# Kernel optimization log

Hardware: AMD Instinct MI355X
Metric: run time of the kernel (lower is better)

Reference implementation:

```python
import jax, jax.numpy as jnp
import numpy as np


def setup_inputs() -> dict:
    key = jax.random.key(0)
    ks = jax.random.split(key, 8)
    B, T, V, H = 32, 256, 1024, 1024
    scale_i = 1.0 / np.sqrt(V)   # lecun_normal-style init for dense kernels
    scale_h = 1.0 / np.sqrt(H)
    return {
        "c0": jax.random.normal(ks[0], (B, H), jnp.float32),
        "h0": jax.random.normal(ks[1], (B, H), jnp.float32),
        "inputs": jax.random.normal(ks[2], (B, T, V), jnp.float32),
        "Wi": jax.random.normal(ks[3], (V, 4 * H), jnp.float32) * scale_i,
        "Wh": jax.random.normal(ks[4], (H, 4 * H), jnp.float32) * scale_h,
        "b": jnp.zeros((4 * H,), jnp.float32),
        "Wd": jax.random.normal(ks[5], (H, V), jnp.float32) * scale_h,
        "bd": jnp.zeros((V,), jnp.float32),
    }


def reference(c0, h0, inputs, Wi, Wh, b, Wd, bd):
    # LSTM scanned over time axis (axis=1 of inputs), then Dense -> vocab.
    H = h0.shape[-1]

    def step(carry, x_t):  # x_t: [B, V]
        c, h = carry
        z = x_t @ Wi + h @ Wh + b            # [B, 4H], gates i,f,g,o
        i, f, g, o = jnp.split(z, 4, axis=-1)
        i = jax.nn.sigmoid(i)
        f = jax.nn.sigmoid(f)
        g = jnp.tanh(g)
        o = jax.nn.sigmoid(o)
        c = f * c + i * g
        h = o * jnp.tanh(c)
        return (c, h), h

    xs = jnp.swapaxes(inputs, 0, 1)          # [T, B, V]
    (c, h), hs = jax.lax.scan(step, (c0, h0), xs)
    outputs = jnp.swapaxes(hs, 0, 1)          # [B, T, H]
    x = outputs @ Wd + bd                     # [B, T, V]
    return (c, h, x)
```

## Files before the change

kernel.cpp:

```cpp
#include <hip/hip_runtime.h>
#include <cstdio>

typedef unsigned short u16;
typedef unsigned int u32;
typedef unsigned long long u64;
typedef __attribute__((ext_vector_type(8))) short bf16x8;
typedef __attribute__((ext_vector_type(4))) float f32x4;

#define NWG 128
#define FLAG_STRIDE 32

__device__ inline u16 f2bf(float x) {
  union { float f; unsigned u; } v; v.f = x;
  unsigned r = v.u + 0x7FFFu + ((v.u >> 16) & 1u);
  return (u16)(r >> 16);
}
__device__ inline float sigm(float x) { return 1.0f / (1.0f + __expf(-x)); }
__device__ inline float tanh_fast(float x) { return 1.0f - 2.0f / (__expf(2.0f * x) + 1.0f); }

__global__ __launch_bounds__(256) void k_convert(const float* __restrict__ in,
                                                 u16* __restrict__ out, int n4) {
  int i = blockIdx.x * blockDim.x + threadIdx.x;
  int stride = gridDim.x * blockDim.x;
  const float4* in4 = (const float4*)in;
  ushort4* out4 = (ushort4*)out;
  for (; i < n4; i += stride) {
    float4 v = in4[i];
    ushort4 o; o.x = f2bf(v.x); o.y = f2bf(v.y); o.z = f2bf(v.z); o.w = f2bf(v.w);
    out4[i] = o;
  }
}

__global__ __launch_bounds__(256) void k_init_h(const float* __restrict__ h0,
                                                u16* __restrict__ h_bf,
                                                u32* __restrict__ flags) {
  int i = blockIdx.x * blockDim.x + threadIdx.x;
  if (i < NWG * FLAG_STRIDE) flags[i] = 0u;
  if (i < 32768) h_bf[i] = f2bf(h0[i]);
}

__global__ __launch_bounds__(256) void k_transpose(const float* __restrict__ in,
                                                   u16* __restrict__ out, int R, int C) {
  __shared__ u16 tile[32][33];
  int tx = threadIdx.x & 31, ty = threadIdx.x >> 5;
  int c = blockIdx.x * 32 + tx;
  for (int i = 0; i < 32; i += 8) {
    int r = blockIdx.y * 32 + ty + i;
    tile[ty + i][tx] = f2bf(in[(size_t)r * C + c]);
  }
  __syncthreads();
  int r = blockIdx.y * 32 + tx;
  for (int i = 0; i < 32; i += 8) {
    int cc = blockIdx.x * 32 + ty + i;
    out[(size_t)cc * R + r] = tile[tx][ty + i];
  }
}

__global__ __launch_bounds__(256) void k_gemm_bt(const u16* __restrict__ A,
                                                 const u16* __restrict__ BT,
                                                 const float* __restrict__ bias,
                                                 float* __restrict__ C,
                                                 int M, int N, int K) {
  __shared__ u16 As[128][40];
  __shared__ u16 Bs[128][40];
  const int m0 = blockIdx.y * 128, n0 = blockIdx.x * 128;
  const int tid = threadIdx.x;
  const int lane = tid & 63, wave = tid >> 6;
  const int wm = (wave >> 1) * 64, wn = (wave & 1) * 64;
  const int lm = lane & 15, quad = lane >> 4;
  const int r = tid >> 1, kh = (tid & 1) * 16;

  f32x4 acc[4][4];
  for (int i = 0; i < 4; i++)
    for (int j = 0; j < 4; j++) acc[i][j] = (f32x4){0.f, 0.f, 0.f, 0.f};

  for (int k0 = 0; k0 < K; k0 += 32) {
    const uint4* ap = (const uint4*)(A + (size_t)(m0 + r) * K + k0 + kh);
    uint4 av0 = ap[0], av1 = ap[1];
    const uint4* bp = (const uint4*)(BT + (size_t)(n0 + r) * K + k0 + kh);
    uint4 bv0 = bp[0], bv1 = bp[1];
    __syncthreads();
    *(uint4*)&As[r][kh] = av0; *(uint4*)&As[r][kh + 8] = av1;
    *(uint4*)&Bs[r][kh] = bv0; *(uint4*)&Bs[r][kh + 8] = bv1;
    __syncthreads();
    bf16x8 a_frag[4], b_frag[4];
    for (int i = 0; i < 4; i++) a_frag[i] = *(const bf16x8*)&As[wm + i * 16 + lm][quad * 8];
    for (int j = 0; j < 4; j++) b_frag[j] = *(const bf16x8*)&Bs[wn + j * 16 + lm][quad * 8];
    for (int i = 0; i < 4; i++)
      for (int j = 0; j < 4; j++)
        acc[i][j] = __builtin_amdgcn_mfma_f32_16x16x32_bf16(a_frag[i], b_frag[j], acc[i][j], 0, 0, 0);
  }
  for (int i = 0; i < 4; i++)
    for (int j = 0; j < 4; j++) {
      int row = m0 + wm + i * 16 + quad * 4;
      int col = n0 + wn + j * 16 + lm;
      float bc = bias[col];
      for (int rr = 0; rr < 4; rr++)
        C[(size_t)(row + rr) * N + col] = acc[i][j][rr] + bc;
    }
}

__global__ __launch_bounds__(256) void k_lstm(const float* __restrict__ Z,
                                              const u16* __restrict__ WhT,
                                              const float* __restrict__ c0,
                                              u16* __restrict__ h_bf,
                                              u16* __restrict__ Hs,
                                              float* __restrict__ out_c,
                                              float* __restrict__ out_h,
                                              u32* __restrict__ flags) {
  __shared__ u16 Whs[32][1032];
  __shared__ u16 h_lds[32][1032];
  __shared__ float z_buf[32][34];
  const int g = blockIdx.x;
  const int tid = threadIdx.x;
  const int lane = tid & 63, wave = tid >> 6;
  const int lm = lane & 15, quad = lane >> 4;
  const int mhalf = wave >> 1, ntile = wave & 1;
  const int b = tid >> 3, jl = tid & 7;

  {
    int pc = tid >> 3, seg = tid & 7;
    int grow = (pc >> 3) * 1024 + 8 * g + (pc & 7);
    const uint4* src = (const uint4*)(WhT + (size_t)grow * 1024 + seg * 128);
#pragma unroll
    for (int i = 0; i < 16; i++) {
      uint4 v = src[i];
      *(uint4*)&Whs[pc][seg * 128 + i * 8] = v;
    }
  }
  float creg = c0[b * 1024 + 8 * g + jl];

  for (int t = 0; t < 256; t++) {
    size_t zbase = ((size_t)b * 256 + t) * 4096 + 8 * g + jl;
    float z_i = Z[zbase], z_f = Z[zbase + 1024], z_g = Z[zbase + 2048], z_o = Z[zbase + 3072];

    {
      const u32 tgt = (u32)t;
      const u32* f0 = flags + lane * FLAG_STRIDE;
      const u32* f1 = flags + (lane + 64) * FLAG_STRIDE;
      while (true) {
        u32 v0 = __hip_atomic_load(f0, __ATOMIC_RELAXED, __HIP_MEMORY_SCOPE_AGENT);
        u32 v1 = __hip_atomic_load(f1, __ATOMIC_RELAXED, __HIP_MEMORY_SCOPE_AGENT);
        if (__all((v0 >= tgt) && (v1 >= tgt))) break;
        __builtin_amdgcn_s_sleep(1);
      }
      asm volatile("" ::: "memory");
    }

    {
      const u64* hq = (const u64*)(h_bf + (size_t)(t & 1) * 32768);
      u64 v[32];
#pragma unroll
      for (int i = 0; i < 32; i++)
        v[i] = __hip_atomic_load(hq + i * 256 + tid, __ATOMIC_RELAXED, __HIP_MEMORY_SCOPE_AGENT);
#pragma unroll
      for (int i = 0; i < 32; i++) {
        int q = i * 256 + tid;
        *(u64*)&h_lds[q >> 8][(q & 255) * 4] = v[i];
      }
    }
    __syncthreads();

    const u16* arow = &h_lds[mhalf * 16 + lm][quad * 8];
    const u16* brow = &Whs[ntile * 16 + lm][quad * 8];
    f32x4 a0 = (f32x4){0.f, 0.f, 0.f, 0.f}, a1 = a0, a2 = a0, a3 = a0;
#pragma unroll
    for (int ks = 0; ks < 32; ks += 4) {
      bf16x8 af0 = *(const bf16x8*)(arow + (ks + 0) * 32);
      bf16x8 bf0 = *(const bf16x8*)(brow + (ks + 0) * 32);
      bf16x8 af1 = *(const bf16x8*)(arow + (ks + 1) * 32);
      bf16x8 bf1 = *(const bf16x8*)(brow + (ks + 1) * 32);
      bf16x8 af2 = *(const bf16x8*)(arow + (ks + 2) * 32);
      bf16x8 bf2 = *(const bf16x8*)(brow + (ks + 2) * 32);
      bf16x8 af3 = *(const bf16x8*)(arow + (ks + 3) * 32);
      bf16x8 bf3 = *(const bf16x8*)(brow + (ks + 3) * 32);
      a0 = __builtin_amdgcn_mfma_f32_16x16x32_bf16(af0, bf0, a0, 0, 0, 0);
      a1 = __builtin_amdgcn_mfma_f32_16x16x32_bf16(af1, bf1, a1, 0, 0, 0);
      a2 = __builtin_amdgcn_mfma_f32_16x16x32_bf16(af2, bf2, a2, 0, 0, 0);
      a3 = __builtin_amdgcn_mfma_f32_16x16x32_bf16(af3, bf3, a3, 0, 0, 0);
    }
    f32x4 accs = (a0 + a1) + (a2 + a3);
    for (int rr = 0; rr < 4; rr++)
      z_buf[mhalf * 16 + quad * 4 + rr][ntile * 16 + lm] = accs[rr];
    __syncthreads();

    float zi = z_buf[b][jl]      + z_i;
    float zf = z_buf[b][8 + jl]  + z_f;
    float zg = z_buf[b][16 + jl] + z_g;
    float zo = z_buf[b][24 + jl] + z_o;
    float ig = sigm(zi), fg = sigm(zf), gg = tanh_fast(zg), og = sigm(zo);
    creg = fg * creg + ig * gg;
    float hv = og * tanh_fast(creg);
    u16 hb = f2bf(hv);
    __hip_atomic_store(h_bf + (size_t)((t + 1) & 1) * 32768 + b * 1024 + 8 * g + jl,
                       hb, __ATOMIC_RELAXED, __HIP_MEMORY_SCOPE_AGENT);
    __builtin_nontemporal_store(hb, Hs + ((size_t)b * 256 + t) * 1024 + 8 * g + jl);
    if (t == 255) {
      out_c[b * 1024 + 8 * g + jl] = creg;
      out_h[b * 1024 + 8 * g + jl] = hv;
    }
    __syncthreads();
    if (tid == 0)
      __hip_atomic_store(flags + g * FLAG_STRIDE, (u32)(t + 1),
                         __ATOMIC_RELAXED, __HIP_MEMORY_SCOPE_AGENT);
  }
}

extern "C" void kernel_launch(void* const* d_in, const int* in_sizes, int n_in,
                              void* d_out, int out_size, void* d_ws, size_t ws_size,
                              hipStream_t stream) {
  const float* c0   = (const float*)d_in[0];
  const float* h0   = (const float*)d_in[1];
  const float* X    = (const float*)d_in[2];
  const float* Wi   = (const float*)d_in[3];
  const float* Wh   = (const float*)d_in[4];
  const float* bias = (const float*)d_in[5];
  const float* Wd   = (const float*)d_in[6];
  const float* bd   = (const float*)d_in[7];
  float* out   = (float*)d_out;
  float* out_c = out;
  float* out_h = out + 32768;
  float* out_x = out + 65536;

  char* ws = (char*)d_ws;
  size_t off = 0;
  auto alloc = [&](size_t bytes) { char* p = ws + off; off += (bytes + 255) & ~255ull; return p; };
  float* Z     = (float*)alloc(134217728ull);
  u16*   Xb    = (u16*)alloc(16777216ull);
  u16*   WiT   = (u16*)alloc(8388608ull);
  u16*   WhT   = (u16*)alloc(8388608ull);
  u16*   WdT   = (u16*)alloc(2097152ull);
  u16*   Hs    = (u16*)alloc(16777216ull);
  u16*   h_bf  = (u16*)alloc(131072ull);
  u32*   flags = (u32*)alloc(NWG * FLAG_STRIDE * 4);
  if (off > ws_size) {
    fprintf(stderr, "WS too small: need %zu have %zu\n", off, ws_size);
    return;
  }

  k_convert<<<2048, 256, 0, stream>>>(X, Xb, 8388608 / 4);
  k_init_h<<<128, 256, 0, stream>>>(h0, h_bf, flags);
  k_transpose<<<dim3(128, 32), 256, 0, stream>>>(Wi, WiT, 1024, 4096);
  k_transpose<<<dim3(128, 32), 256, 0, stream>>>(Wh, WhT, 1024, 4096);
  k_transpose<<<dim3(32, 32), 256, 0, stream>>>(Wd, WdT, 1024, 1024);
  k_gemm_bt<<<dim3(32, 64), 256, 0, stream>>>(Xb, WiT, bias, Z, 8192, 4096, 1024);
  k_lstm<<<NWG, 256, 0, stream>>>(Z, WhT, c0, h_bf, Hs, out_c, out_h, flags);
  k_gemm_bt<<<dim3(8, 64), 256, 0, stream>>>(Hs, WdT, bd, out_x, 8192, 1024, 1024);
}
```

Before: 1.178 ms.

## Replace flag barrier with sentinel-polled per-step hidden-state buffers in persistent LSTM

Removes the per-step global flag barrier. Each timestep now writes h into its own slot of a 257-step buffer that is pre-filled with a bf16 sentinel (+inf), and consumers spin on the loaded h words until no sentinel remains. The Wh slice is kept in registers instead of LDS, h fragments are read straight from global into MFMA operands, and the K dimension is split across waves with a double-buffered LDS reduction, which drops one __syncthreads per step. The cost is an extra clear kernel over the reused Xb workspace. The scheme assumes a real h value never equals the sentinel and relies on relaxed-atomic visibility.

```diff
diff --git a/kernel.cpp b/kernel.cpp
--- a/kernel.cpp
+++ b/kernel.cpp
@@ -8,7 +8,8 @@
 typedef __attribute__((ext_vector_type(4))) float f32x4;
 
 #define NWG 128
-#define FLAG_STRIDE 32
+#define SENT16 0x7F80u
+#define SENT32 0x7F807F80u
 
 __device__ inline u16 f2bf(float x) {
   union { float f; unsigned u; } v; v.f = x;
@@ -17,6 +18,11 @@
 }
 __device__ inline float sigm(float x) { return 1.0f / (1.0f + __expf(-x)); }
 __device__ inline float tanh_fast(float x) { return 1.0f - 2.0f / (__expf(2.0f * x) + 1.0f); }
+__device__ inline bool badw(u64 v) {
+  u32 a = (u32)v, b = (u32)(v >> 32);
+  return ((a & 0xffffu) == SENT16) | ((a >> 16) == SENT16) |
+         ((b & 0xffffu) == SENT16) | ((b >> 16) == SENT16);
+}
 
 __global__ __launch_bounds__(256) void k_convert(const float* __restrict__ in,
                                                  u16* __restrict__ out, int n4) {
@@ -31,12 +37,17 @@
   }
 }
 
+__global__ __launch_bounds__(256) void k_clear(uint4* __restrict__ p, int n) {
+  int i = blockIdx.x * blockDim.x + threadIdx.x;
+  int stride = gridDim.x * blockDim.x;
+  uint4 s = make_uint4(SENT32, SENT32, SENT32, SENT32);
+  for (; i < n; i += stride) p[i] = s;
+}
+
 __global__ __launch_bounds__(256) void k_init_h(const float* __restrict__ h0,
-                                                u16* __restrict__ h_bf,
-                                                u32* __restrict__ flags) {
+                                                u16* __restrict__ hseq) {
   int i = blockIdx.x * blockDim.x + threadIdx.x;
-  if (i < NWG * FLAG_STRIDE) flags[i] = 0u;
-  if (i < 32768) h_bf[i] = f2bf(h0[i]);
+  if (i < 32768) hseq[i] = f2bf(h0[i]);
 }
 
 __global__ __launch_bounds__(256) void k_transpose(const float* __restrict__ in,
@@ -100,109 +111,91 @@
     }
 }
 
-__global__ __launch_bounds__(256) void k_lstm(const float* __restrict__ Z,
-                                              const u16* __restrict__ WhT,
-                                              const float* __restrict__ c0,
-                                              u16* __restrict__ h_bf,
-                                              u16* __restrict__ Hs,
-                                              float* __restrict__ out_c,
-                                              float* __restrict__ out_h,
-                                              u32* __restrict__ flags) {
-  __shared__ u16 Whs[32][1032];
-  __shared__ u16 h_lds[32][1032];
-  __shared__ float z_buf[32][34];
+__global__ __launch_bounds__(256, 1) void k_lstm(const float* __restrict__ Z,
+                                                 const u16* __restrict__ WhT,
+                                                 const float* __restrict__ c0,
+                                                 u16* __restrict__ hseq,
+                                                 u16* __restrict__ Hs,
+                                                 float* __restrict__ out_c,
+                                                 float* __restrict__ out_h) {
+  __shared__ float z_buf[2][2][32][34];
   const int g = blockIdx.x;
   const int tid = threadIdx.x;
   const int lane = tid & 63, wave = tid >> 6;
   const int lm = lane & 15, quad = lane >> 4;
-  const int mhalf = wave >> 1, ntile = wave & 1;
+  const int mhalf = wave & 1, khalf = wave >> 1;
   const int b = tid >> 3, jl = tid & 7;
 
+  bf16x8 wf0[16], wf1[16];
   {
-    int pc = tid >> 3, seg = tid & 7;
-    int grow = (pc >> 3) * 1024 + 8 * g + (pc & 7);
-    const uint4* src = (const uint4*)(WhT + (size_t)grow * 1024 + seg * 128);
-#pragma unroll
-    for (int i = 0; i < 16; i++) {
-      uint4 v = src[i];
-      *(uint4*)&Whs[pc][seg * 128 + i * 8] = v;
+    int pc0 = lm, pc1 = 16 + lm;
+    const u16* w0 = WhT + (size_t)((pc0 >> 3) * 1024 + 8 * g + (pc0 & 7)) * 1024 + khalf * 512 + quad * 8;
+    const u16* w1 = WhT + (size_t)((pc1 >> 3) * 1024 + 8 * g + (pc1 & 7)) * 1024 + khalf * 512 + quad * 8;
+#pragma unroll
+    for (int ks = 0; ks < 16; ks++) {
+      wf0[ks] = *(const bf16x8*)(w0 + ks * 32);
+      wf1[ks] = *(const bf16x8*)(w1 + ks * 32);
     }
   }
   float creg = c0[b * 1024 + 8 * g + jl];
+
+  const size_t aoff_u64 = (((size_t)(mhalf * 16 + lm) * 1024) + khalf * 512 + quad * 8) >> 2;
 
   for (int t = 0; t < 256; t++) {
     size_t zbase = ((size_t)b * 256 + t) * 4096 + 8 * g + jl;
     float z_i = Z[zbase], z_f = Z[zbase + 1024], z_g = Z[zbase + 2048], z_o = Z[zbase + 3072];
 
-    {
-      const u32 tgt = (u32)t;
-      const u32* f0 = flags + lane * FLAG_STRIDE;
-      const u32* f1 = flags + (lane + 64) * FLAG_STRIDE;
-      while (true) {
-        u32 v0 = __hip_atomic_load(f0, __ATOMIC_RELAXED, __HIP_MEMORY_SCOPE_AGENT);
-        u32 v1 = __hip_atomic_load(f1, __ATOMIC_RELAXED, __HIP_MEMORY_SCOPE_AGENT);
-        if (__all((v0 >= tgt) && (v1 >= tgt))) break;
-        __builtin_amdgcn_s_sleep(1);
+    const u64* hq = (const u64*)hseq + (size_t)t * 8192 + aoff_u64;
+    u64 lo[16], hi[16];
+#pragma unroll
+    for (int i = 0; i < 16; i++) {
+      lo[i] = __hip_atomic_load(hq + i * 8,     __ATOMIC_RELAXED, __HIP_MEMORY_SCOPE_AGENT);
+      hi[i] = __hip_atomic_load(hq + i * 8 + 1, __ATOMIC_RELAXED, __HIP_MEMORY_SCOPE_AGENT);
+    }
+    while (true) {
+      int bad = 0;
+#pragma unroll
+      for (int i = 0; i < 16; i++) {
+        if (badw(lo[i])) { lo[i] = __hip_atomic_load(hq + i * 8,     __ATOMIC_RELAXED, __HIP_MEMORY_SCOPE_AGENT); bad = 1; }
+        if (badw(hi[i])) { hi[i] = __hip_atomic_load(hq + i * 8 + 1, __ATOMIC_RELAXED, __HIP_MEMORY_SCOPE_AGENT); bad = 1; }
       }
-      asm volatile("" ::: "memory");
-    }
-
-    {
-      const u64* hq = (const u64*)(h_bf + (size_t)(t & 1) * 32768);
-      u64 v[32];
-#pragma unroll
-      for (int i = 0; i < 32; i++)
-        v[i] = __hip_atomic_load(hq + i * 256 + tid, __ATOMIC_RELAXED, __HIP_MEMORY_SCOPE_AGENT);
-#pragma unroll
-      for (int i = 0; i < 32; i++) {
-        int q = i * 256 + tid;
-        *(u64*)&h_lds[q >> 8][(q & 255) * 4] = v[i];
-      }
+      if (!__any(bad)) break;
+    }
+
+    f32x4 a0e = (f32x4){0.f, 0.f, 0.f, 0.f}, a0o = a0e, a1e = a0e, a1o = a0e;
+#pragma unroll
+    for (int ks = 0; ks < 16; ks += 2) {
+      union { u64 q[2]; bf16x8 v; } f0, f1;
+      f0.q[0] = lo[ks];     f0.q[1] = hi[ks];
+      f1.q[0] = lo[ks + 1]; f1.q[1] = hi[ks + 1];
+      a0e = __builtin_amdgcn_mfma_f32_16x16x32_bf16(f0.v, wf0[ks],     a0e, 0, 0, 0);
+      a1e = __builtin_amdgcn_mfma_f32_16x16x32_bf16(f0.v, wf1[ks],     a1e, 0, 0, 0);
+      a0o = __builtin_amdgcn_mfma_f32_16x16x32_bf16(f1.v, wf0[ks + 1], a0o, 0, 0, 0);
+      a1o = __builtin_amdgcn_mfma_f32_16x16x32_bf16(f1.v, wf1[ks + 1], a1o, 0, 0, 0);
+    }
+    f32x4 zt0 = a0e + a0o, zt1 = a1e + a1o;
+    const int par = t & 1;
+    for (int rr = 0; rr < 4; rr++) {
+      z_buf[par][khalf][mhalf * 16 + quad * 4 + rr][lm]      = zt0[rr];
+      z_buf[par][khalf][mhalf * 16 + quad * 4 + rr][16 + lm] = zt1[rr];
     }
     __syncthreads();
 
-    const u16* arow = &h_lds[mhalf * 16 + lm][quad * 8];
-    const u16* brow = &Whs[ntile * 16 + lm][quad * 8];
-    f32x4 a0 = (f32x4){0.f, 0.f, 0.f, 0.f}, a1 = a0, a2 = a0, a3 = a0;
-#pragma unroll
-    for (int ks = 0; ks < 32; ks += 4) {
-      bf16x8 af0 = *(const bf16x8*)(arow + (ks + 0) * 32);
-      bf16x8 bf0 = *(const bf16x8*)(brow + (ks + 0) * 32);
-      bf16x8 af1 = *(const bf16x8*)(arow + (ks + 1) * 32);
-      bf16x8 bf1 = *(const bf16x8*)(brow + (ks + 1) * 32);
-      bf16x8 af2 = *(const bf16x8*)(arow + (ks + 2) * 32);
-      bf16x8 bf2 = *(const bf16x8*)(brow + (ks + 2) * 32);
-      bf16x8 af3 = *(const bf16x8*)(arow + (ks + 3) * 32);
-      bf16x8 bf3 = *(const bf16x8*)(brow + (ks + 3) * 32);
-      a0 = __builtin_amdgcn_mfma_f32_16x16x32_bf16(af0, bf0, a0, 0, 0, 0);
-      a1 = __builtin_amdgcn_mfma_f32_16x16x32_bf16(af1, bf1, a1, 0, 0, 0);
-      a2 = __builtin_amdgcn_mfma_f32_16x16x32_bf16(af2, bf2, a2, 0, 0, 0);
-      a3 = __builtin_amdgcn_mfma_f32_16x16x32_bf16(af3, bf3, a3, 0, 0, 0);
-    }
-    f32x4 accs = (a0 + a1) + (a2 + a3);
-    for (int rr = 0; rr < 4; rr++)
-      z_buf[mhalf * 16 + quad * 4 + rr][ntile * 16 + lm] = accs[rr];
-    __syncthreads();
-
-    float zi = z_buf[b][jl]      + z_i;
-    float zf = z_buf[b][8 + jl]  + z_f;
-    float zg = z_buf[b][16 + jl] + z_g;
-    float zo = z_buf[b][24 + jl] + z_o;
+    float zi = z_buf[par][0][b][jl]      + z_buf[par][1][b][jl]      + z_i;
+    float zf = z_buf[par][0][b][8 + jl]  + z_buf[par][1][b][8 + jl]  + z_f;
+    float zg = z_buf[par][0][b][16 + jl] + z_buf[par][1][b][16 + jl] + z_g;
+    float zo = z_buf[par][0][b][24 + jl] + z_buf[par][1][b][24 + jl] + z_o;
     float ig = sigm(zi), fg = sigm(zf), gg = tanh_fast(zg), og = sigm(zo);
     creg = fg * creg + ig * gg;
     float hv = og * tanh_fast(creg);
     u16 hb = f2bf(hv);
-    __hip_atomic_store(h_bf + (size_t)((t + 1) & 1) * 32768 + b * 1024 + 8 * g + jl,
+    __hip_atomic_store(hseq + (size_t)(t + 1) * 32768 + b * 1024 + 8 * g + jl,
                        hb, __ATOMIC_RELAXED, __HIP_MEMORY_SCOPE_AGENT);
     __builtin_nontemporal_store(hb, Hs + ((size_t)b * 256 + t) * 1024 + 8 * g + jl);
     if (t == 255) {
       out_c[b * 1024 + 8 * g + jl] = creg;
       out_h[b * 1024 + 8 * g + jl] = hv;
     }
-    __syncthreads();
-    if (tid == 0)
-      __hip_atomic_store(flags + g * FLAG_STRIDE, (u32)(t + 1),
-                         __ATOMIC_RELAXED, __HIP_MEMORY_SCOPE_AGENT);
   }
 }
 
@@ -225,25 +218,26 @@
   char* ws = (char*)d_ws;
   size_t off = 0;
   auto alloc = [&](size_t bytes) { char* p = ws + off; off += (bytes + 255) & ~255ull; return p; };
-  float* Z     = (float*)alloc(134217728ull);
-  u16*   Xb    = (u16*)alloc(16777216ull);
-  u16*   WiT   = (u16*)alloc(8388608ull);
-  u16*   WhT   = (u16*)alloc(8388608ull);
-  u16*   WdT   = (u16*)alloc(2097152ull);
-  u16*   Hs    = (u16*)alloc(16777216ull);
-  u16*   h_bf  = (u16*)alloc(131072ull);
-  u32*   flags = (u32*)alloc(NWG * FLAG_STRIDE * 4);
+  float* Z   = (float*)alloc(134217728ull);
+  u16*   Xb  = (u16*)alloc(16777216ull);
+  u16*   WiT = (u16*)alloc(8388608ull);
+  u16*   WhT = (u16*)alloc(8388608ull);
+  u16*   WdT = (u16*)alloc(2097152ull);
+  u16*   Hs  = (u16*)alloc(16777216ull);
+  u16*   hseq = Xb;
+  const int hseq_u16 = 257 * 32768;
   if (off > ws_size) {
     fprintf(stderr, "WS too small: need %zu have %zu\n", off, ws_size);
     return;
   }
 
   k_convert<<<2048, 256, 0, stream>>>(X, Xb, 8388608 / 4);
-  k_init_h<<<128, 256, 0, stream>>>(h0, h_bf, flags);
   k_transpose<<<dim3(128, 32), 256, 0, stream>>>(Wi, WiT, 1024, 4096);
   k_transpose<<<dim3(128, 32), 256, 0, stream>>>(Wh, WhT, 1024, 4096);
   k_transpose<<<dim3(32, 32), 256, 0, stream>>>(Wd, WdT, 1024, 1024);
   k_gemm_bt<<<dim3(32, 64), 256, 0, stream>>>(Xb, WiT, bias, Z, 8192, 4096, 1024);
-  k_lstm<<<NWG, 256, 0, stream>>>(Z, WhT, c0, h_bf, Hs, out_c, out_h, flags);
+  k_clear<<<2048, 256, 0, stream>>>((uint4*)hseq, hseq_u16 / 8);
+  k_init_h<<<128, 256, 0, stream>>>(h0, hseq);
+  k_lstm<<<NWG, 256, 0, stream>>>(Z, WhT, c0, hseq, Hs, out_c, out_h);
   k_gemm_bt<<<dim3(8, 64), 256, 0, stream>>>(Hs, WdT, bd, out_x, 8192, 1024, 1024);
 }
```

Result: slower. 2.383 ms (+102.3%).
